# Optimization experiments

Hardware: AMD Instinct MI355X
Metric: run time of the kernel (lower is better)

Reference implementation:

```python
import jax, jax.numpy as jnp
import numpy as np

D_IN, D_K, D_V, N_HEADS = 1024, 64, 64, 16
B, S = 4, 2048


def setup_inputs() -> dict:
    key = jax.random.key(0)
    ks = jax.random.split(key, 9)
    scale = 1.0 / np.sqrt(D_IN)
    return {
        "X": jax.random.normal(ks[0], (B, S, D_IN), dtype=jnp.float32),
        # per-head projection weights, stacked over heads: [H, d_in, d]
        "Wq": jax.random.normal(ks[1], (N_HEADS, D_IN, D_K), dtype=jnp.float32) * scale,
        "bq": jax.random.normal(ks[2], (N_HEADS, D_K), dtype=jnp.float32) * 0.02,
        "Wk": jax.random.normal(ks[3], (N_HEADS, D_IN, D_K), dtype=jnp.float32) * scale,
        "bk": jax.random.normal(ks[4], (N_HEADS, D_K), dtype=jnp.float32) * 0.02,
        "Wv": jax.random.normal(ks[5], (N_HEADS, D_IN, D_V), dtype=jnp.float32) * scale,
        "bv": jax.random.normal(ks[6], (N_HEADS, D_V), dtype=jnp.float32) * 0.02,
        # output projection: [H*d_v, d_in]
        "Wo": jax.random.normal(ks[7], (N_HEADS * D_V, D_IN), dtype=jnp.float32) * (1.0 / np.sqrt(N_HEADS * D_V)),
        "bo": jax.random.normal(ks[8], (D_IN,), dtype=jnp.float32) * 0.02,
    }


def reference(X, Wq, bq, Wk, bk, Wv, bv, Wo, bo):
    # Per-head linear projections, all heads batched: [B,H,S,d]
    Q = jnp.einsum('bsd,hdk->bhsk', X, Wq) + bq[None, :, None, :]
    K = jnp.einsum('bsd,hdk->bhsk', X, Wk) + bk[None, :, None, :]
    V = jnp.einsum('bsd,hdv->bhsv', X, Wv) + bv[None, :, None, :]

    d_k = Q.shape[-1]
    scores = jnp.einsum('bhsk,bhtk->bhst', Q, K) / jnp.sqrt(jnp.float32(d_k))

    S_len = X.shape[1]
    causal = jnp.tril(jnp.ones((S_len, S_len), dtype=bool))  # [S,S]
    scores = jnp.where(causal[None, None, :, :], scores, -jnp.inf)
    P = jax.nn.softmax(scores, axis=-1)

    A = jnp.einsum('bhst,bhtv->bhsv', P, V)        # [B,H,S,d_v]
    # concat heads along feature dim (head-major order matches torch cat over heads)
    A = A.transpose(0, 2, 1, 3).reshape(X.shape[0], S_len, -1)  # [B,S,H*d_v]
    return A @ Wo + bo
```

## Files before the change

### kernel.cpp

```cpp
#include <hip/hip_runtime.h>
#include <cstdint>
#include <cstddef>

typedef __attribute__((ext_vector_type(4))) float f32x4;
typedef __attribute__((ext_vector_type(8))) short s16x8;
typedef __attribute__((ext_vector_type(4))) short s16x4;
typedef __attribute__((ext_vector_type(4))) int i32x4;

#define DEV __device__ __forceinline__

DEV short f2bf(float f) {
    unsigned u = __builtin_bit_cast(unsigned, f);
    unsigned r = (u + 0x7FFFu + ((u >> 16) & 1u)) >> 16;
    return (short)r;
}

DEV void gload_lds16(const void* g, void* l) {
    __builtin_amdgcn_global_load_lds(
        (const __attribute__((address_space(1))) unsigned int*)g,
        (__attribute__((address_space(3))) unsigned int*)l, 16, 0, 0);
}


__global__ void k_cvt_x(const float* __restrict__ X, short* __restrict__ Xb, int n4) {
    int stride = gridDim.x * blockDim.x;
    for (int i = blockIdx.x * blockDim.x + threadIdx.x; i < n4; i += stride) {
        f32x4 v = *(const f32x4*)&X[i * 4];
        s16x4 s;
#pragma unroll
        for (int j = 0; j < 4; ++j) s[j] = f2bf(v[j]);
        *(s16x4*)&Xb[i * 4] = s;
    }
}

__global__ void k_pack_wqkv(const float* __restrict__ Wq, const float* __restrict__ Wk,
                            const float* __restrict__ Wv, short* __restrict__ Wbt, int n) {
    int stride = gridDim.x * blockDim.x;
    for (int o = blockIdx.x * blockDim.x + threadIdx.x; o < n; o += stride) {
        int c = o >> 10, d = o & 1023;
        int t = c >> 10, h = (c >> 6) & 15, k = c & 63;
        const float* W = (t == 0) ? Wq : (t == 1) ? Wk : Wv;
        Wbt[o] = f2bf(W[(h * 1024 + d) * 64 + k]);
    }
}

__global__ void k_pack_wo(const float* __restrict__ Wo, short* __restrict__ Wobt, int n) {
    int stride = gridDim.x * blockDim.x;
    for (int o = blockIdx.x * blockDim.x + threadIdx.x; o < n; o += stride) {
        int nn = o >> 10, c = o & 1023;
        Wobt[o] = f2bf(Wo[c * 1024 + nn]);
    }
}


template <int EPI>
__launch_bounds__(256)
__global__ void gemm_bf16(const short* __restrict__ Ag, const short* __restrict__ Btg,
                          const float* __restrict__ b0, const float* __restrict__ b1,
                          const float* __restrict__ b2,
                          short* __restrict__ O0, short* __restrict__ O1, short* __restrict__ O2,
                          float* __restrict__ Of) {
    __shared__ short As[128 * 64];
    __shared__ short Bs[128 * 64];
    const int tid = threadIdx.x;
    const int wave = tid >> 6, lane = tid & 63;
    const int wm = wave >> 1, wn = wave & 1;
    const int m0 = blockIdx.y * 128, n0 = blockIdx.x * 128;

    f32x4 acc[4][4] = {};

    const int lr = lane >> 3;
    const int cb = (lane & 7) * 16;
    const int cl = cb ^ (lr << 4);

    for (int kt = 0; kt < 16; ++kt) {
        __syncthreads();
#pragma unroll
        for (int i = 0; i < 4; ++i) {
            int r8 = wave * 32 + i * 8;
            const char* ga = (const char*)(Ag + (size_t)(m0 + r8 + lr) * 1024 + kt * 64) + cl;
            gload_lds16(ga, &As[r8 * 64]);
            const char* gb = (const char*)(Btg + (size_t)(n0 + r8 + lr) * 1024 + kt * 64) + cl;
            gload_lds16(gb, &Bs[r8 * 64]);
        }
        asm volatile("s_waitcnt vmcnt(0)" ::: "memory");
        __syncthreads();
#pragma unroll
        for (int ks = 0; ks < 2; ++ks) {
            int kb = ks * 64 + (lane >> 4) * 16;
            s16x8 af[4], bf[4];
#pragma unroll
            for (int mf = 0; mf < 4; ++mf) {
                int m = wm * 64 + mf * 16 + (lane & 15);
                af[mf] = *(const s16x8*)&As[m * 64 + ((kb ^ ((m & 7) << 4)) >> 1)];
            }
#pragma unroll
            for (int nf = 0; nf < 4; ++nf) {
                int n = wn * 64 + nf * 16 + (lane & 15);
                bf[nf] = *(const s16x8*)&Bs[n * 64 + ((kb ^ ((n & 7) << 4)) >> 1)];
            }
#pragma unroll
            for (int mf = 0; mf < 4; ++mf)
#pragma unroll
                for (int nf = 0; nf < 4; ++nf)
                    acc[mf][nf] = __builtin_amdgcn_mfma_f32_16x16x32_bf16(af[mf], bf[nf],
                                                                          acc[mf][nf], 0, 0, 0);
        }
    }

    if (EPI == 0) {
#pragma unroll
        for (int nf = 0; nf < 4; ++nf) {
            int n = n0 + wn * 64 + nf * 16 + (lane & 15);
            int t = n >> 10;
            int h = (n >> 6) & 15;
            int kk = n & 63;
            const float* bias = (t == 0) ? b0 : (t == 1) ? b1 : b2;
            short* dst = (t == 0) ? O0 : (t == 1) ? O1 : O2;
            float scale = (t == 0) ? 0.1803368851f : 1.0f;
            float bb = bias[h * 64 + kk];
#pragma unroll
            for (int mf = 0; mf < 4; ++mf) {
#pragma unroll
                for (int r = 0; r < 4; ++r) {
                    int m = m0 + wm * 64 + mf * 16 + (lane >> 4) * 4 + r;
                    int b_ = m >> 11, sp = m & 2047;
                    float v = (acc[mf][nf][r] + bb) * scale;
                    dst[(((size_t)(b_ * 16 + h)) * 2048 + sp) * 64 + kk] = f2bf(v);
                }
            }
        }
    } else {
#pragma unroll
        for (int nf = 0; nf < 4; ++nf) {
            int n = n0 + wn * 64 + nf * 16 + (lane & 15);
            float bb = b0[n];
#pragma unroll
            for (int mf = 0; mf < 4; ++mf) {
#pragma unroll
                for (int r = 0; r < 4; ++r) {
                    int m = m0 + wm * 64 + mf * 16 + (lane >> 4) * 4 + r;
                    Of[(size_t)m * 1024 + n] = acc[mf][nf][r] + bb;
                }
            }
        }
    }
}


#define STAGE_K(KT, OFF) do {                                                   \
    _Pragma("unroll")                                                           \
    for (int i_ = 0; i_ < 2; ++i_) {                                            \
        int l_ = wave * 16 + i_ * 8 + lr;          \
        int gr_ = (((l_ >> 4) & 1) << 5) | (((l_ >> 2) & 3) << 3) |             \
                  (((l_ >> 5) & 1) << 2) | (l_ & 3);        \
        const char* g_ = (const char*)(Kb + base + (size_t)((KT) * 64 + gr_) * 64) + cl; \
        gload_lds16(g_, &KsAll[(OFF) + (wave * 16 + i_ * 8) * 64]);             \
    } } while (0)

#define LOAD_V(KT) do {                                                         \
    const short* vs_ = Vb + base + (size_t)((KT) * 64 + 2 * kp) * 64 + vb8 * 8; \
    v0_ = *(const s16x8*)vs_;                                                   \
    v1_ = *(const s16x8*)(vs_ + 64); } while (0)

#define WRITE_V(OFF) do {                                                       \
    _Pragma("unroll")                                                           \
    for (int j_ = 0; j_ < 8; ++j_) {                                            \
        int v_ = vb8 * 8 + j_;                                                  \
        unsigned pk_ = (unsigned)(unsigned short)v0_[j_] |                      \
                       ((unsigned)(unsigned short)v1_[j_] << 16);               \
        int bo_ = (4 * kp) ^ ((v_ & 7) << 4);                                   \
        *(unsigned*)((char*)&VtAll[(OFF) + v_ * 64] + bo_) = pk_;               \
    } } while (0)

#define STRIP2_COMPUTE(KT, OFF) do {                                            \
    f32x4 scL_[4], scS_[4];                                                     \
    _Pragma("unroll")                                                           \
    for (int nf_ = 0; nf_ < 4; ++nf_)                                           \
        _Pragma("unroll")                                                       \
        for (int r_ = 0; r_ < 4; ++r_) { scL_[nf_][r_] = -10.f; scS_[nf_][r_] = -10.f; } \
    __builtin_amdgcn_s_setprio(1);                                              \
    _Pragma("unroll")                                                           \
    for (int ks_ = 0; ks_ < 2; ++ks_) {                                         \
        int kb_ = ks_ * 64 + (lane >> 4) * 16;                                  \
        _Pragma("unroll")                                                       \
        for (int nf_ = 0; nf_ < 4; ++nf_) {                                     \
            int key_ = nf_ * 16 + (lane & 15);                                  \
            s16x8 bf_ = *(const s16x8*)&KsAll[(OFF) + key_ * 64 + ((kb_ ^ ((key_ & 7) << 4)) >> 1)]; \
            scL_[nf_] = __builtin_amdgcn_mfma_f32_16x16x32_bf16(bf_, qL_[ks_], scL_[nf_], 0, 0, 0); \
            scS_[nf_] = __builtin_amdgcn_mfma_f32_16x16x32_bf16(bf_, qS_[ks_], scS_[nf_], 0, 0, 0); \
        }                                                                       \
    }                                                                           \
    __builtin_amdgcn_s_setprio(0);                                              \
    if ((KT) == QTSv_) {                                   \
        int qq_ = wave * 16 + (lane & 15);                                      \
        int g8_ = (lane >> 4) * 8;                                              \
        _Pragma("unroll")                                                       \
        for (int nf_ = 0; nf_ < 4; ++nf_) {                                     \
            _Pragma("unroll")                                                   \
            for (int r_ = 0; r_ < 4; ++r_) {                                    \
                int key_ = ((nf_ & 1) << 5) + g8_ + ((nf_ >> 1) << 2) + r_;     \
                if (key_ > qq_) scS_[nf_][r_] = NEG_INF;                        \
            }                                                                   \
        }                                                                       \
    }                                                                           \
    _Pragma("unroll")                                                           \
    for (int nf_ = 0; nf_ < 4; ++nf_)                                           \
        _Pragma("unroll")                                                       \
        for (int r_ = 0; r_ < 4; ++r_) {                                        \
            scL_[nf_][r_] = exp2f(scL_[nf_][r_]);                               \
            scS_[nf_][r_] = exp2f(scS_[nf_][r_]);                               \
        }                                                                       \
    unsigned pdL_[4][2], pdS_[4][2];                                            \
    _Pragma("unroll")                                                           \
    for (int nf_ = 0; nf_ < 4; ++nf_) {                                         \
        asm("v_cvt_pk_bf16_f32 %0, %1, %2"                                      \
            : "=v"(pdL_[nf_][0]) : "v"(scL_[nf_][0]), "v"(scL_[nf_][1]));       \
        asm("v_cvt_pk_bf16_f32 %0, %1, %2"                                      \
            : "=v"(pdL_[nf_][1]) : "v"(scL_[nf_][2]), "v"(scL_[nf_][3]));       \
        asm("v_cvt_pk_bf16_f32 %0, %1, %2"                                      \
            : "=v"(pdS_[nf_][0]) : "v"(scS_[nf_][0]), "v"(scS_[nf_][1]));       \
        asm("v_cvt_pk_bf16_f32 %0, %1, %2"                                      \
            : "=v"(pdS_[nf_][1]) : "v"(scS_[nf_][2]), "v"(scS_[nf_][3]));       \
    }                                                                           \
    __builtin_amdgcn_s_setprio(1);                                              \
    _Pragma("unroll")                                                           \
    for (int ks_ = 0; ks_ < 2; ++ks_) {                                         \
        i32x4 piL_, piS_;                                                       \
        piL_[0] = (int)pdL_[ks_][0]; piL_[1] = (int)pdL_[ks_][1];               \
        piL_[2] = (int)pdL_[ks_ + 2][0]; piL_[3] = (int)pdL_[ks_ + 2][1];       \
        piS_[0] = (int)pdS_[ks_][0]; piS_[1] = (int)pdS_[ks_][1];               \
        piS_[2] = (int)pdS_[ks_ + 2][0]; piS_[3] = (int)pdS_[ks_ + 2][1];       \
        s16x8 paL_ = __builtin_bit_cast(s16x8, piL_);                           \
        s16x8 paS_ = __builtin_bit_cast(s16x8, piS_);                           \
        lsumL_ = __builtin_amdgcn_mfma_f32_16x16x32_bf16(paL_, onesf, lsumL_, 0, 0, 0); \
        lsumS_ = __builtin_amdgcn_mfma_f32_16x16x32_bf16(paS_, onesf, lsumS_, 0, 0, 0); \
        int kb_ = ks_ * 64 + (lane >> 4) * 16;                                  \
        _Pragma("unroll")                                                       \
        for (int nf_ = 0; nf_ < 4; ++nf_) {                                     \
            int v_ = nf_ * 16 + (lane & 15);                                    \
            s16x8 vf_ = *(const s16x8*)&VtAll[(OFF) + v_ * 64 + ((kb_ ^ ((v_ & 7) << 4)) >> 1)]; \
            oL_[nf_] = __builtin_amdgcn_mfma_f32_16x16x32_bf16(paL_, vf_, oL_[nf_], 0, 0, 0); \
            oS_[nf_] = __builtin_amdgcn_mfma_f32_16x16x32_bf16(paS_, vf_, oS_[nf_], 0, 0, 0); \
        }                                                                       \
    }                                                                           \
    __builtin_amdgcn_s_setprio(0);                                              \
    } while (0)

#define STRIP_COMPUTE(QF, O, LSUM, KT, OFF) do {                                \
    f32x4 sc_[4];                                                               \
    _Pragma("unroll")                                                           \
    for (int nf_ = 0; nf_ < 4; ++nf_)                                           \
        _Pragma("unroll")                                                       \
        for (int r_ = 0; r_ < 4; ++r_) sc_[nf_][r_] = -10.f;                    \
    __builtin_amdgcn_s_setprio(1);                                              \
    _Pragma("unroll")                                                           \
    for (int ks_ = 0; ks_ < 2; ++ks_) {                                         \
        int kb_ = ks_ * 64 + (lane >> 4) * 16;                                  \
        _Pragma("unroll")                                                       \
        for (int nf_ = 0; nf_ < 4; ++nf_) {                                     \
            int key_ = nf_ * 16 + (lane & 15);                                  \
            s16x8 bf_ = *(const s16x8*)&KsAll[(OFF) + key_ * 64 + ((kb_ ^ ((key_ & 7) << 4)) >> 1)]; \
            sc_[nf_] = __builtin_amdgcn_mfma_f32_16x16x32_bf16(bf_, QF[ks_], sc_[nf_], 0, 0, 0); \
        }                                                                       \
    }                                                                           \
    __builtin_amdgcn_s_setprio(0);                                              \
    {                                                                           \
        int qq_ = wave * 16 + (lane & 15);                                      \
        int g8_ = (lane >> 4) * 8;                                              \
        _Pragma("unroll")                                                       \
        for (int nf_ = 0; nf_ < 4; ++nf_) {                                     \
            _Pragma("unroll")                                                   \
            for (int r_ = 0; r_ < 4; ++r_) {                                    \
                int key_ = ((nf_ & 1) << 5) + g8_ + ((nf_ >> 1) << 2) + r_;     \
                if (key_ > qq_) sc_[nf_][r_] = NEG_INF;                         \
            }                                                                   \
        }                                                                       \
    }                                                                           \
    _Pragma("unroll")                                                           \
    for (int nf_ = 0; nf_ < 4; ++nf_)                                           \
        _Pragma("unroll")                                                       \
        for (int r_ = 0; r_ < 4; ++r_) sc_[nf_][r_] = exp2f(sc_[nf_][r_]);      \
    unsigned pd_[4][2];                                                         \
    _Pragma("unroll")                                                           \
    for (int nf_ = 0; nf_ < 4; ++nf_) {                                         \
        asm("v_cvt_pk_bf16_f32 %0, %1, %2"                                      \
            : "=v"(pd_[nf_][0]) : "v"(sc_[nf_][0]), "v"(sc_[nf_][1]));          \
        asm("v_cvt_pk_bf16_f32 %0, %1, %2"                                      \
            : "=v"(pd_[nf_][1]) : "v"(sc_[nf_][2]), "v"(sc_[nf_][3]));          \
    }                                                                           \
    __builtin_amdgcn_s_setprio(1);                                              \
    _Pragma("unroll")                                                           \
    for (int ks_ = 0; ks_ < 2; ++ks_) {                                         \
        i32x4 pi_;                                                              \
        pi_[0] = (int)pd_[ks_][0]; pi_[1] = (int)pd_[ks_][1];                   \
        pi_[2] = (int)pd_[ks_ + 2][0]; pi_[3] = (int)pd_[ks_ + 2][1];           \
        s16x8 pa_ = __builtin_bit_cast(s16x8, pi_);                             \
        LSUM = __builtin_amdgcn_mfma_f32_16x16x32_bf16(pa_, onesf, LSUM, 0, 0, 0); \
        int kb_ = ks_ * 64 + (lane >> 4) * 16;                                  \
        _Pragma("unroll")                                                       \
        for (int nf_ = 0; nf_ < 4; ++nf_) {                                     \
            int v_ = nf_ * 16 + (lane & 15);                                    \
            s16x8 vf_ = *(const s16x8*)&VtAll[(OFF) + v_ * 64 + ((kb_ ^ ((v_ & 7) << 4)) >> 1)]; \
            O[nf_] = __builtin_amdgcn_mfma_f32_16x16x32_bf16(pa_, vf_, O[nf_], 0, 0, 0); \
        }                                                                       \
    }                                                                           \
    __builtin_amdgcn_s_setprio(0);                                              \
    } while (0)

#define ITERB(T) do {                                                           \
    STAGE_K((T) + 1, off1_);                                                    \
    LOAD_V((T) + 1);                                                            \
    STRIP2_COMPUTE((T), off0_);                                                 \
    asm volatile("s_waitcnt vmcnt(0)" ::: "memory");                            \
    WRITE_V(off1_);                                                             \
    asm volatile("s_waitcnt lgkmcnt(0)" ::: "memory");                          \
    __builtin_amdgcn_s_barrier();                                               \
    int tmp_ = off0_; off0_ = off1_; off1_ = tmp_;                              \
} while (0)

#define EPILOGUE(QT, O, LSUM) do {                                              \
    _Pragma("unroll")                                                           \
    for (int r_ = 0; r_ < 4; ++r_) {                                            \
        float ld_ = 1.0f / LSUM[r_];                                            \
        int qr_ = wave * 16 + (lane >> 4) * 4 + r_;                             \
        _Pragma("unroll")                                                       \
        for (int nf_ = 0; nf_ < 4; ++nf_) {                                     \
            int col_ = h * 64 + nf_ * 16 + (lane & 15);                         \
            Ab[((size_t)(b_ * 2048 + (QT) * 64 + qr_)) * 1024 + col_] =         \
                f2bf(O[nf_][r_] * ld_);                                         \
        }                                                                       \
    } } while (0)

__launch_bounds__(256)
__global__ void attn_fwd(const short* __restrict__ Qb, const short* __restrict__ Kb,
                         const short* __restrict__ Vb, short* __restrict__ Ab) {
    __shared__ short KsAll[2 * 64 * 64];
    __shared__ short VtAll[2 * 64 * 64];
    const int tid = threadIdx.x, wave = tid >> 6, lane = tid & 63;
    const int hx = blockIdx.x;
    const int j = 15 - (int)blockIdx.y;
    const int QTLv_ = 2 * j + 1, QTSv_ = 2 * j;
    const int ntp_ = 2 * j + 2;
    const int NB_ = ntp_ - 1;
    const size_t base = (size_t)hx * 2048 * 64;
    const float NEG_INF = -__builtin_inff();
    const int b_ = hx >> 4, h = hx & 15;

    const int qrow = wave * 16 + (lane & 15);
    const int qoff = (lane >> 4) * 8;
    const int lr = lane >> 3, cl = ((lane & 7) * 16) ^ (lr << 4);
    const int kp = tid & 31;
    const int vb8 = tid >> 5;

    const s16x8 onesf = {(short)0x3F80, (short)0x3F80, (short)0x3F80, (short)0x3F80,
                         (short)0x3F80, (short)0x3F80, (short)0x3F80, (short)0x3F80};

    s16x8 qL_[2], qS_[2];
#pragma unroll
    for (int ks = 0; ks < 2; ++ks) {
        qL_[ks] = *(const s16x8*)&Qb[base + (size_t)(QTLv_ * 64 + qrow) * 64 + ks * 32 + qoff];
        qS_[ks] = *(const s16x8*)&Qb[base + (size_t)(QTSv_ * 64 + qrow) * 64 + ks * 32 + qoff];
    }

    f32x4 oL_[4] = {}, oS_[4] = {};
    f32x4 lsumL_ = {}, lsumS_ = {};
    s16x8 v0_, v1_;
    int off0_ = 0, off1_ = 4096;

    STAGE_K(0, off0_);
    LOAD_V(0);
    asm volatile("s_waitcnt vmcnt(0)" ::: "memory");
    WRITE_V(off0_);
    asm volatile("s_waitcnt lgkmcnt(0)" ::: "memory");
    __builtin_amdgcn_s_barrier();

    for (int t_ = 0; t_ < NB_; ++t_) {
        ITERB(t_);
    }

    STRIP_COMPUTE(qL_, oL_, lsumL_, QTLv_, off0_);

    EPILOGUE(QTLv_, oL_, lsumL_);
    EPILOGUE(QTSv_, oS_, lsumS_);
}


extern "C" void kernel_launch(void* const* d_in, const int* in_sizes, int n_in,
                              void* d_out, int out_size, void* d_ws, size_t ws_size,
                              hipStream_t stream) {
    const float* X  = (const float*)d_in[0];
    const float* Wq = (const float*)d_in[1];
    const float* bq = (const float*)d_in[2];
    const float* Wk = (const float*)d_in[3];
    const float* bk = (const float*)d_in[4];
    const float* Wv = (const float*)d_in[5];
    const float* bv = (const float*)d_in[6];
    const float* Wo = (const float*)d_in[7];
    const float* bo = (const float*)d_in[8];
    float* out = (float*)d_out;
    char* ws = (char*)d_ws;

    short* Xb   = (short*)(ws);
    short* Wbt  = (short*)(ws + 16777216);
    short* Wobt = (short*)(ws + 23068672);
    short* Qb   = (short*)(ws + 25165824);
    short* Kb   = (short*)(ws + 41943040);
    short* Vb   = (short*)(ws + 58720256);
    short* Ab   = (short*)(ws + 75497472);

    k_cvt_x<<<2048, 256, 0, stream>>>(X, Xb, 8192 * 1024 / 4);
    k_pack_wqkv<<<2048, 256, 0, stream>>>(Wq, Wk, Wv, Wbt, 3 * 1024 * 1024);
    k_pack_wo<<<1024, 256, 0, stream>>>(Wo, Wobt, 1024 * 1024);

    gemm_bf16<0><<<dim3(24, 64), 256, 0, stream>>>(Xb, Wbt, bq, bk, bv, Qb, Kb, Vb, nullptr);
    attn_fwd<<<dim3(64, 16), 256, 0, stream>>>(Qb, Kb, Vb, Ab);
    gemm_bf16<1><<<dim3(8, 64), 256, 0, stream>>>(Ab, Wobt, bo, nullptr, nullptr,
                                                  nullptr, nullptr, nullptr, out);
}
```

Measured before the change: 196.8 us.

## Split attention KV range across two blocks and add combine kernel; tile weight transposes

```diff
diff --git a/kernel.cpp b/kernel.cpp
--- a/kernel.cpp
+++ b/kernel.cpp
@@ -13,6 +13,10 @@
     unsigned u = __builtin_bit_cast(unsigned, f);
     unsigned r = (u + 0x7FFFu + ((u >> 16) & 1u)) >> 16;
     return (short)r;
+}
+
+DEV float bf2f(short s) {
+    return __builtin_bit_cast(float, ((unsigned)(unsigned short)s) << 16);
 }
 
 DEV void gload_lds16(const void* g, void* l) {
@@ -33,23 +37,57 @@
     }
 }
 
-__global__ void k_pack_wqkv(const float* __restrict__ Wq, const float* __restrict__ Wk,
-                            const float* __restrict__ Wv, short* __restrict__ Wbt, int n) {
-    int stride = gridDim.x * blockDim.x;
-    for (int o = blockIdx.x * blockDim.x + threadIdx.x; o < n; o += stride) {
-        int c = o >> 10, d = o & 1023;
-        int t = c >> 10, h = (c >> 6) & 15, k = c & 63;
-        const float* W = (t == 0) ? Wq : (t == 1) ? Wk : Wv;
-        Wbt[o] = f2bf(W[(h * 1024 + d) * 64 + k]);
-    }
-}
-
-__global__ void k_pack_wo(const float* __restrict__ Wo, short* __restrict__ Wobt, int n) {
-    int stride = gridDim.x * blockDim.x;
-    for (int o = blockIdx.x * blockDim.x + threadIdx.x; o < n; o += stride) {
-        int nn = o >> 10, c = o & 1023;
-        Wobt[o] = f2bf(Wo[c * 1024 + nn]);
-    }
+__global__ void k_pack_wqkv_t(const float* __restrict__ Wq, const float* __restrict__ Wk,
+                              const float* __restrict__ Wv, short* __restrict__ Wbt) {
+    __shared__ float tileT[64][65];
+    const int bx = blockIdx.x, tid = threadIdx.x;
+    const int t = bx >> 8, h = (bx >> 4) & 15, dc = bx & 15;
+    const float* W = (t == 0) ? Wq : (t == 1) ? Wk : Wv;
+    const float* src = W + ((size_t)h * 1024 + dc * 64) * 64;
+#pragma unroll
+    for (int i = 0; i < 4; ++i) {
+        int idx4 = i * 256 + tid;
+        f32x4 v = *(const f32x4*)&src[idx4 * 4];
+        int flat = idx4 * 4;
+        int d = flat >> 6, k0 = flat & 63;
+#pragma unroll
+        for (int q = 0; q < 4; ++q) tileT[k0 + q][d] = v[q];
+    }
+    __syncthreads();
+    const int k = tid >> 2, d4 = (tid & 3) * 16;
+    s16x8 o0, o1;
+#pragma unroll
+    for (int q = 0; q < 8; ++q) {
+        o0[q] = f2bf(tileT[k][d4 + q]);
+        o1[q] = f2bf(tileT[k][d4 + 8 + q]);
+    }
+    size_t c = (size_t)t * 1024 + h * 64 + k;
+    *(s16x8*)&Wbt[c * 1024 + dc * 64 + d4] = o0;
+    *(s16x8*)&Wbt[c * 1024 + dc * 64 + d4 + 8] = o1;
+}
+
+__global__ void k_pack_wo_t(const float* __restrict__ Wo, short* __restrict__ Wobt) {
+    __shared__ float tileT[64][65];
+    const int bx = blockIdx.x, tid = threadIdx.x;
+    const int c0 = (bx >> 4) * 64, n0 = (bx & 15) * 64;
+    const int r = tid >> 2, cch = tid & 3;
+#pragma unroll
+    for (int it = 0; it < 4; ++it) {
+        int colf = cch * 4 + it * 16;
+        f32x4 v = *(const f32x4*)&Wo[(size_t)(c0 + r) * 1024 + n0 + colf];
+#pragma unroll
+        for (int q = 0; q < 4; ++q) tileT[colf + q][r] = v[q];
+    }
+    __syncthreads();
+    const int n = tid >> 2, c4 = (tid & 3) * 16;
+    s16x8 o0, o1;
+#pragma unroll
+    for (int q = 0; q < 8; ++q) {
+        o0[q] = f2bf(tileT[n][c4 + q]);
+        o1[q] = f2bf(tileT[n][c4 + 8 + q]);
+    }
+    *(s16x8*)&Wobt[(size_t)(n0 + n) * 1024 + c0 + c4] = o0;
+    *(s16x8*)&Wobt[(size_t)(n0 + n) * 1024 + c0 + c4 + 8] = o1;
 }
 
 
@@ -247,7 +285,7 @@
     __builtin_amdgcn_s_setprio(0);                                              \
     } while (0)
 
-#define STRIP_COMPUTE(QF, O, LSUM, KT, OFF) do {                                \
+#define STRIP_COMPUTE(QF, O, LSUM, OFF) do {                                    \
     f32x4 sc_[4];                                                               \
     _Pragma("unroll")                                                           \
     for (int nf_ = 0; nf_ < 4; ++nf_)                                           \
@@ -309,43 +347,44 @@
     } while (0)
 
 #define ITERB(T) do {                                                           \
-    STAGE_K((T) + 1, off1_);                                                    \
-    LOAD_V((T) + 1);                                                            \
+    const bool st_ = ((T) + 1 < hi_);                                           \
+    if (st_) { STAGE_K((T) + 1, off1_); LOAD_V((T) + 1); }                      \
     STRIP2_COMPUTE((T), off0_);                                                 \
     asm volatile("s_waitcnt vmcnt(0)" ::: "memory");                            \
-    WRITE_V(off1_);                                                             \
+    if (st_) WRITE_V(off1_);                                                    \
     asm volatile("s_waitcnt lgkmcnt(0)" ::: "memory");                          \
     __builtin_amdgcn_s_barrier();                                               \
     int tmp_ = off0_; off0_ = off1_; off1_ = tmp_;                              \
 } while (0)
 
-#define EPILOGUE(QT, O, LSUM) do {                                              \
+#define PEPILOGUE(SOFF, O, LSUM) do {                                           \
     _Pragma("unroll")                                                           \
     for (int r_ = 0; r_ < 4; ++r_) {                                            \
-        float ld_ = 1.0f / LSUM[r_];                                            \
-        int qr_ = wave * 16 + (lane >> 4) * 4 + r_;                             \
-        _Pragma("unroll")                                                       \
-        for (int nf_ = 0; nf_ < 4; ++nf_) {                                     \
-            int col_ = h * 64 + nf_ * 16 + (lane & 15);                         \
-            Ab[((size_t)(b_ * 2048 + (QT) * 64 + qr_)) * 1024 + col_] =         \
-                f2bf(O[nf_][r_] * ld_);                                         \
-        }                                                                       \
+        int row_ = (SOFF) + wave * 16 + (lane >> 4) * 4 + r_;                   \
+        if ((lane & 15) == 0) Lp_[row_] = LSUM[r_];                             \
+        _Pragma("unroll")                                                       \
+        for (int nf_ = 0; nf_ < 4; ++nf_)                                       \
+            Op_[row_ * 64 + nf_ * 16 + (lane & 15)] = f2bf(O[nf_][r_]);         \
     } } while (0)
 
 __launch_bounds__(256)
 __global__ void attn_fwd(const short* __restrict__ Qb, const short* __restrict__ Kb,
-                         const short* __restrict__ Vb, short* __restrict__ Ab) {
+                         const short* __restrict__ Vb, short* __restrict__ Opart,
+                         float* __restrict__ Lpart) {
     __shared__ short KsAll[2 * 64 * 64];
     __shared__ short VtAll[2 * 64 * 64];
     const int tid = threadIdx.x, wave = tid >> 6, lane = tid & 63;
     const int hx = blockIdx.x;
-    const int j = 15 - (int)blockIdx.y;
-    const int QTLv_ = 2 * j + 1, QTSv_ = 2 * j;
-    const int ntp_ = 2 * j + 2;
-    const int NB_ = ntp_ - 1;
+    const int y = blockIdx.y;
+    const int jj = 15 - (y >> 1);
+    const int half = y & 1;
+    const int lo_ = half * (jj + 1);
+    const int hi_ = lo_ + jj + 1;
+    const int QTSv_ = 2 * jj, QTLv_ = 2 * jj + 1;
+    const int ND_ = ((hi_ < QTLv_) ? hi_ : QTLv_) - lo_;
+    const bool tail_ = (hi_ > QTLv_);
     const size_t base = (size_t)hx * 2048 * 64;
     const float NEG_INF = -__builtin_inff();
-    const int b_ = hx >> 4, h = hx & 15;
 
     const int qrow = wave * 16 + (lane & 15);
     const int qoff = (lane >> 4) * 8;
@@ -368,21 +407,50 @@
     s16x8 v0_, v1_;
     int off0_ = 0, off1_ = 4096;
 
-    STAGE_K(0, off0_);
-    LOAD_V(0);
+    STAGE_K(lo_, off0_);
+    LOAD_V(lo_);
     asm volatile("s_waitcnt vmcnt(0)" ::: "memory");
     WRITE_V(off0_);
     asm volatile("s_waitcnt lgkmcnt(0)" ::: "memory");
     __builtin_amdgcn_s_barrier();
 
-    for (int t_ = 0; t_ < NB_; ++t_) {
+    for (int t_ = lo_; t_ < lo_ + ND_; ++t_) {
         ITERB(t_);
     }
-
-    STRIP_COMPUTE(qL_, oL_, lsumL_, QTLv_, off0_);
-
-    EPILOGUE(QTLv_, oL_, lsumL_);
-    EPILOGUE(QTSv_, oS_, lsumS_);
+    if (tail_) {
+        STRIP_COMPUTE(qL_, oL_, lsumL_, off0_);
+    }
+
+    const int slot_ = (hx * 16 + jj) * 2 + half;
+    short* Op_ = Opart + (size_t)slot_ * 8192;
+    float* Lp_ = Lpart + (size_t)slot_ * 128;
+    PEPILOGUE(0, oS_, lsumS_);
+    PEPILOGUE(64, oL_, lsumL_);
+}
+
+__launch_bounds__(256)
+__global__ void attn_combine(const short* __restrict__ Opart, const float* __restrict__ Lpart,
+                             short* __restrict__ Ab) {
+    const int bx = blockIdx.x, t = threadIdx.x;
+    const int hx = bx >> 4, jj = bx & 15;
+    const int b_ = hx >> 4, h = hx & 15;
+    const short* O0 = Opart + (size_t)((hx * 16 + jj) * 2) * 8192;
+    const short* O1 = O0 + 8192;
+    const float* L0 = Lpart + (size_t)((hx * 16 + jj) * 2) * 128;
+    const float* L1 = L0 + 128;
+    const int c4 = (t & 15) * 4;
+#pragma unroll
+    for (int p = 0; p < 8; ++p) {
+        int row = (t >> 4) + p * 16;
+        float rl = 1.0f / (L0[row] + L1[row]);
+        s16x4 a = *(const s16x4*)&O0[row * 64 + c4];
+        s16x4 b = *(const s16x4*)&O1[row * 64 + c4];
+        s16x4 o;
+#pragma unroll
+        for (int q = 0; q < 4; ++q) o[q] = f2bf((bf2f(a[q]) + bf2f(b[q])) * rl);
+        int qglob = jj * 128 + row;
+        *(s16x4*)&Ab[((size_t)(b_ * 2048 + qglob)) * 1024 + h * 64 + c4] = o;
+    }
 }
 
 
@@ -401,20 +469,23 @@
     float* out = (float*)d_out;
     char* ws = (char*)d_ws;
 
-    short* Xb   = (short*)(ws);
-    short* Wbt  = (short*)(ws + 16777216);
-    short* Wobt = (short*)(ws + 23068672);
-    short* Qb   = (short*)(ws + 25165824);
-    short* Kb   = (short*)(ws + 41943040);
-    short* Vb   = (short*)(ws + 58720256);
-    short* Ab   = (short*)(ws + 75497472);
+    short* Wobt  = (short*)(ws);
+    short* Qb    = (short*)(ws + 2097152);
+    short* Kb    = (short*)(ws + 18874368);
+    short* Vb    = (short*)(ws + 35651584);
+    short* Ab    = (short*)(ws + 52428800);
+    short* Xb    = (short*)(ws + 69206016);
+    short* Wbt   = (short*)(ws + 85983232);
+    short* Opart = (short*)(ws + 69206016);
+    float* Lpart = (float*)(ws + 102760448);
 
     k_cvt_x<<<2048, 256, 0, stream>>>(X, Xb, 8192 * 1024 / 4);
-    k_pack_wqkv<<<2048, 256, 0, stream>>>(Wq, Wk, Wv, Wbt, 3 * 1024 * 1024);
-    k_pack_wo<<<1024, 256, 0, stream>>>(Wo, Wobt, 1024 * 1024);
+    k_pack_wqkv_t<<<768, 256, 0, stream>>>(Wq, Wk, Wv, Wbt);
+    k_pack_wo_t<<<256, 256, 0, stream>>>(Wo, Wobt);
 
     gemm_bf16<0><<<dim3(24, 64), 256, 0, stream>>>(Xb, Wbt, bq, bk, bv, Qb, Kb, Vb, nullptr);
-    attn_fwd<<<dim3(64, 16), 256, 0, stream>>>(Qb, Kb, Vb, Ab);
+    attn_fwd<<<dim3(64, 32), 256, 0, stream>>>(Qb, Kb, Vb, Opart, Lpart);
+    attn_combine<<<1024, 256, 0, stream>>>(Opart, Lpart, Ab);
     gemm_bf16<1><<<dim3(8, 64), 256, 0, stream>>>(Ab, Wobt, bo, nullptr, nullptr,
                                                   nullptr, nullptr, nullptr, out);
 }
```

New measurement: 189.7 us. 3.6% less time.
